# Kernel tuning notes

Measured on AMD Instinct MI355X. Metric: run time of the kernel, lower is better.

The kernel has to match this reference:

```python
import jax, jax.numpy as jnp
import numpy as np

B, S, D = 2, 4096, 2048
HQ, HK, HV = 32, 8, 8
H = max(HQ, HK, HV)
DK, DV = 64, 64
OUT = 2048
CHUNK = 64  # chunked-recurrent block size


def setup_inputs() -> dict:
    key = jax.random.key(0)
    k1, k2, k3 = jax.random.split(key, 3)
    x = jax.random.normal(k1, (B, S, D), dtype=jnp.float32)
    input_state = jnp.zeros((B, H * DK * DV), dtype=jnp.float32)
    qkv = HQ * DK + HK * DK + HV * DV  # 3072
    # Linear weights stored as [in, out]; equals torch weight.T so y = x @ W
    W_in = jax.random.normal(k2, (D, qkv), dtype=jnp.float32) * (D ** -0.5)
    W_out = jax.random.normal(k3, (H * DV, OUT), dtype=jnp.float32) * ((H * DV) ** -0.5)
    return {"x": x, "input_state": input_state, "W_in": W_in, "W_out": W_out}


def _linear_attention(q, k, v, S0):
    # q,k,v: [B,S,H,d]; S0: [B,H,DK,DV]
    nc = S // CHUNK
    # move chunk axis to front for lax.scan: [nc, B, CHUNK, H, d]
    qc = jnp.moveaxis(q.reshape(B, nc, CHUNK, H, DK), 1, 0)
    kc = jnp.moveaxis(k.reshape(B, nc, CHUNK, H, DK), 1, 0)
    vc = jnp.moveaxis(v.reshape(B, nc, CHUNK, H, DV), 1, 0)
    mask = jnp.tril(jnp.ones((CHUNK, CHUNK), dtype=bool))  # causal within chunk

    def step(Sstate, blk):
        qb, kb, vb = blk  # [B,C,H,d]
        A = jnp.einsum('bihd,bjhd->bhij', qb, kb)
        A = jnp.where(mask, A, jnp.zeros((), A.dtype))
        o = jnp.einsum('bhij,bjhd->bihd', A, vb) \
            + jnp.einsum('bihd,bhde->bihe', qb, Sstate)
        Sstate = Sstate + jnp.einsum('bjhd,bjhe->bhde', kb, vb)
        return Sstate, o

    Sf, o = jax.lax.scan(step, S0, (qc, kc, vc))
    o = jnp.moveaxis(o, 0, 1).reshape(B, S, H, DV)
    return o, Sf


def reference(x, input_state, W_in, W_out):
    proj = x @ W_in  # [B,S,3072]
    q, k, v = jnp.split(proj, [HQ * DK, HQ * DK + HK * DK], axis=-1)
    q = q.reshape(B, S, HQ, DK)
    k = k.reshape(B, S, HK, DK)
    v = v.reshape(B, S, HV, DV)
    # GQA: repeat kv heads up to num_heads = max(...)
    k = jnp.repeat(k, H // HK, axis=2)
    v = jnp.repeat(v, H // HV, axis=2)
    S0 = input_state.reshape(B, H, DK, DV)
    o, Sf = _linear_attention(q, k, v, S0)
    out = o.reshape(B, S, H * DV) @ W_out
    return out, Sf.reshape(B, H, DK * DV)
```

## Files before the change

kernel.cpp:

```cpp
#include <hip/hip_runtime.h>

typedef __bf16 bf16_t;
typedef __bf16 bf16x8 __attribute__((ext_vector_type(8)));
typedef __bf16 bf16x4 __attribute__((ext_vector_type(4)));
typedef float  f32x4  __attribute__((ext_vector_type(4)));

#define MFMA16(a,b,c) __builtin_amdgcn_mfma_f32_16x16x32_bf16((a),(b),(c),0,0,0)

__device__ __forceinline__ void gl_lds16(const void* g, void* l) {
    __builtin_amdgcn_global_load_lds(
        (__attribute__((address_space(1))) void*)(g),
        (__attribute__((address_space(3))) void*)(l),
        16, 0, 0);
}

static constexpr int S_TOT   = 8192;
static constexpr int D_IN    = 2048;
static constexpr int QKV     = 3072;
static constexpr int OUT_D   = 2048;
static constexpr int NCHUNK  = 64;

__global__ __launch_bounds__(256)
void cvt_f32_bf16(const float* __restrict__ in, bf16_t* __restrict__ out) {
    int i = blockIdx.x * 256 + threadIdx.x;
    f32x4 v = ((const f32x4*)in)[i];
    bf16x4 o;
    o[0] = (bf16_t)v[0]; o[1] = (bf16_t)v[1]; o[2] = (bf16_t)v[2]; o[3] = (bf16_t)v[3];
    ((bf16x4*)out)[i] = o;
}

__global__ __launch_bounds__(256)
void transpose_f32_bf16(const float* __restrict__ in, bf16_t* __restrict__ out, int R, int C) {
    __shared__ float tile[64][65];
    const int t  = threadIdx.x;
    const int r0 = blockIdx.y * 64, c0 = blockIdx.x * 64;
#pragma unroll
    for (int p = 0; p < 4; p++) {
        int row = p * 16 + (t >> 4);
        int col = (t & 15) * 4;
        f32x4 v = *(const f32x4*)&in[(size_t)(r0 + row) * C + c0 + col];
        tile[row][col + 0] = v[0]; tile[row][col + 1] = v[1];
        tile[row][col + 2] = v[2]; tile[row][col + 3] = v[3];
    }
    __syncthreads();
#pragma unroll
    for (int p = 0; p < 4; p++) {
        int oc  = p * 16 + (t >> 4);
        int orr = (t & 15) * 4;
        bf16x4 v;
        v[0] = (bf16_t)tile[orr + 0][oc]; v[1] = (bf16_t)tile[orr + 1][oc];
        v[2] = (bf16_t)tile[orr + 2][oc]; v[3] = (bf16_t)tile[orr + 3][oc];
        *(bf16x4*)&out[(size_t)(c0 + oc) * R + r0 + orr] = v;
    }
}

template<int OUT_BF16>
__global__ __launch_bounds__(256)
void gemm_bt(const bf16_t* __restrict__ A, const bf16_t* __restrict__ Bt,
             void* __restrict__ Cout, int M, int N, int K) {
    __shared__ alignas(16) bf16_t lA[128 * 32];
    __shared__ alignas(16) bf16_t lB[128 * 32];
    const int tid = threadIdx.x;
    const int m0 = blockIdx.y * 128;
    const int n0 = blockIdx.x * 128;
    const int w = tid >> 6, lane = tid & 63;
    const int wr = (w >> 1) * 64, wc = (w & 1) * 64;
    const int l15 = lane & 15, q8 = (lane >> 4) * 8, q4 = (lane >> 4) * 4;
    f32x4 acc[4][4] = {};
    const bf16_t* Ag = A + (size_t)(m0 + (tid >> 2)) * K + (tid & 3) * 8;
    const bf16_t* Bg = Bt + (size_t)(n0 + (tid >> 2)) * K + (tid & 3) * 8;
    const size_t rowStep = (size_t)64 * K;
    bf16_t* lA_t = lA + tid * 8;
    bf16_t* lB_t = lB + tid * 8;
    for (int k0 = 0; k0 < K; k0 += 32) {
        gl_lds16(Ag + k0,           lA_t);
        gl_lds16(Ag + k0 + rowStep, lA_t + 64 * 32);
        gl_lds16(Bg + k0,           lB_t);
        gl_lds16(Bg + k0 + rowStep, lB_t + 64 * 32);
        __syncthreads();
        bf16x8 af[4], bf_[4];
#pragma unroll
        for (int mi = 0; mi < 4; mi++) af[mi]  = *(const bf16x8*)&lA[(wr + mi * 16 + l15) * 32 + q8];
#pragma unroll
        for (int nj = 0; nj < 4; nj++) bf_[nj] = *(const bf16x8*)&lB[(wc + nj * 16 + l15) * 32 + q8];
#pragma unroll
        for (int mi = 0; mi < 4; mi++)
#pragma unroll
            for (int nj = 0; nj < 4; nj++)
                acc[mi][nj] = MFMA16(af[mi], bf_[nj], acc[mi][nj]);
        __syncthreads();
    }
    if (OUT_BF16) {
        bf16_t* C = (bf16_t*)Cout;
#pragma unroll
        for (int mi = 0; mi < 4; mi++)
#pragma unroll
            for (int nj = 0; nj < 4; nj++)
#pragma unroll
                for (int r = 0; r < 4; r++)
                    C[(size_t)(m0 + wr + mi * 16 + q4 + r) * N + n0 + wc + nj * 16 + l15] =
                        (bf16_t)acc[mi][nj][r];
    } else {
        float* C = (float*)Cout;
#pragma unroll
        for (int mi = 0; mi < 4; mi++)
#pragma unroll
            for (int nj = 0; nj < 4; nj++)
#pragma unroll
                for (int r = 0; r < 4; r++)
                    C[(size_t)(m0 + wr + mi * 16 + q4 + r) * N + n0 + wc + nj * 16 + l15] =
                        acc[mi][nj][r];
    }
}

__global__ __launch_bounds__(64)
void chunk_kv(const bf16_t* __restrict__ proj, float* __restrict__ Zc) {
    const int idx = blockIdx.x;
    const int c = idx & 63, hk = (idx >> 6) & 7, b = idx >> 9;
    const int tokBase = b * 4096 + c * 64;
    __shared__ alignas(16) bf16_t kT[64 * 64];
    __shared__ alignas(16) bf16_t vT[64 * 64];
    const int lane = threadIdx.x;
    const bf16_t* kg = proj + (size_t)tokBase * QKV + 2048 + hk * 64;
    const bf16_t* vg = proj + (size_t)tokBase * QKV + 2560 + hk * 64;
#pragma unroll
    for (int p = 0; p < 8; p++) {
        int tok = p * 8 + (lane >> 3);
        int d0  = (lane & 7) * 8;
        bf16x8 kv = *(const bf16x8*)&kg[(size_t)tok * QKV + d0];
        bf16x8 vv = *(const bf16x8*)&vg[(size_t)tok * QKV + d0];
#pragma unroll
        for (int e = 0; e < 8; e++) {
            kT[(d0 + e) * 64 + tok] = kv[e];
            vT[(d0 + e) * 64 + tok] = vv[e];
        }
    }
    __syncthreads();
    const int l15 = lane & 15, q8 = (lane >> 4) * 8, q4 = (lane >> 4) * 4;
    f32x4 acc[4][4] = {};
#pragma unroll
    for (int ks = 0; ks < 2; ks++) {
        bf16x8 af[4], bf_[4];
#pragma unroll
        for (int mi = 0; mi < 4; mi++) af[mi]  = *(const bf16x8*)&vT[(mi * 16 + l15) * 64 + ks * 32 + q8];
#pragma unroll
        for (int nj = 0; nj < 4; nj++) bf_[nj] = *(const bf16x8*)&kT[(nj * 16 + l15) * 64 + ks * 32 + q8];
#pragma unroll
        for (int mi = 0; mi < 4; mi++)
#pragma unroll
            for (int nj = 0; nj < 4; nj++)
                acc[mi][nj] = MFMA16(af[mi], bf_[nj], acc[mi][nj]);
    }
    float* zout = Zc + (size_t)idx * 4096;
#pragma unroll
    for (int mi = 0; mi < 4; mi++)
#pragma unroll
        for (int nj = 0; nj < 4; nj++)
#pragma unroll
            for (int r = 0; r < 4; r++)
                zout[(mi * 16 + q4 + r) * 64 + nj * 16 + l15] = acc[mi][nj][r];
}

__global__ __launch_bounds__(256)
void prefix_state(const float* __restrict__ Zc, const float* __restrict__ S0,
                  bf16_t* __restrict__ Zp, float* __restrict__ SfOut) {
    const int slice = blockIdx.x & 15;
    const int bh = blockIdx.x >> 4;
    const int h = bh & 31, b = bh >> 5;
    const int hk = h >> 2;
    const int e = slice * 256 + threadIdx.x;
    const int dv = e >> 6, dk = e & 63;
    float acc = S0[(size_t)b * 131072 + h * 4096 + dk * 64 + dv];
    const float* zc = Zc + ((size_t)(b * 8 + hk) * 64) * 4096 + e;
    bf16_t* zp = Zp + ((size_t)(b * 32 + h) * 64) * 4096 + e;
    for (int c = 0; c < NCHUNK; c++) {
        zp[(size_t)c * 4096] = (bf16_t)acc;
        acc += zc[(size_t)c * 4096];
    }
    SfOut[(size_t)b * 131072 + h * 4096 + dk * 64 + dv] = acc;
}

__global__ __launch_bounds__(64)
void attn_chunk(const bf16_t* __restrict__ proj, const bf16_t* __restrict__ Zp,
                bf16_t* __restrict__ O) {
    const int idx = blockIdx.x;
    const int g = idx & 3, hk = (idx >> 2) & 7, c = (idx >> 5) & 63, b = idx >> 11;
    const int h = hk * 4 + g;
    const int tokBase = b * 4096 + c * 64;
    __shared__ alignas(16) bf16_t q_lds[64 * 64];
    __shared__ alignas(16) bf16_t k_lds[64 * 64];
    __shared__ alignas(16) bf16_t vT[64 * 64];
    __shared__ alignas(16) bf16_t zs[64 * 64];
    const int lane = threadIdx.x;
    const bf16_t* qg = proj + (size_t)tokBase * QKV + h * 64;
    const bf16_t* kg = proj + (size_t)tokBase * QKV + 2048 + hk * 64;
    const bf16_t* zg = Zp + (((size_t)(b * 32 + h)) * 64 + c) * 4096;
#pragma unroll
    for (int p = 0; p < 8; p++) {
        int row = p * 8 + (lane >> 3);
        int col = (lane & 7) * 8;
        gl_lds16(&qg[(size_t)row * QKV + col], &q_lds[p * 512 + lane * 8]);
        gl_lds16(&kg[(size_t)row * QKV + col], &k_lds[p * 512 + lane * 8]);
        gl_lds16(&zg[p * 512 + lane * 8],      &zs[p * 512 + lane * 8]);
    }
    const bf16_t* vg = proj + (size_t)tokBase * QKV + 2560 + hk * 64;
#pragma unroll
    for (int p = 0; p < 8; p++) {
        int tok = p * 8 + (lane >> 3);
        int d0  = (lane & 7) * 8;
        bf16x8 vv = *(const bf16x8*)&vg[(size_t)tok * QKV + d0];
#pragma unroll
        for (int e = 0; e < 8; e++) vT[(d0 + e) * 64 + tok] = vv[e];
    }
    __syncthreads();
    const int l15 = lane & 15, q8 = (lane >> 4) * 8, q4 = (lane >> 4) * 4;
    bf16x8 qf[2][4];
#pragma unroll
    for (int ks = 0; ks < 2; ks++)
#pragma unroll
        for (int mi = 0; mi < 4; mi++)
            qf[ks][mi] = *(const bf16x8*)&q_lds[(mi * 16 + l15) * 64 + ks * 32 + q8];
    f32x4 oacc[4][4] = {};
#pragma unroll
    for (int ks = 0; ks < 2; ks++) {
        bf16x8 zf[4];
#pragma unroll
        for (int nj = 0; nj < 4; nj++) zf[nj] = *(const bf16x8*)&zs[(nj * 16 + l15) * 64 + ks * 32 + q8];
#pragma unroll
        for (int mi = 0; mi < 4; mi++)
#pragma unroll
            for (int nj = 0; nj < 4; nj++)
                oacc[mi][nj] = MFMA16(qf[ks][mi], zf[nj], oacc[mi][nj]);
    }
    f32x4 sacc[4][4] = {};
#pragma unroll
    for (int ks = 0; ks < 2; ks++) {
        bf16x8 kf[4];
#pragma unroll
        for (int nj = 0; nj < 4; nj++) kf[nj] = *(const bf16x8*)&k_lds[(nj * 16 + l15) * 64 + ks * 32 + q8];
#pragma unroll
        for (int mi = 0; mi < 4; mi++)
#pragma unroll
            for (int nj = 0; nj < 4; nj++)
                if (mi >= nj) sacc[mi][nj] = MFMA16(qf[ks][mi], kf[nj], sacc[mi][nj]);
    }
    __syncthreads();
#pragma unroll
    for (int mi = 0; mi < 4; mi++)
#pragma unroll
        for (int nj = 0; nj < 4; nj++)
#pragma unroll
            for (int r = 0; r < 4; r++) {
                int ti = mi * 16 + q4 + r, tj = nj * 16 + l15;
                float v = (ti >= tj) ? sacc[mi][nj][r] : 0.0f;
                zs[ti * 64 + tj] = (bf16_t)v;
            }
    __syncthreads();
#pragma unroll
    for (int ks = 0; ks < 2; ks++) {
        bf16x8 sf[4], vf[4];
#pragma unroll
        for (int mi = 0; mi < 4; mi++) sf[mi] = *(const bf16x8*)&zs[(mi * 16 + l15) * 64 + ks * 32 + q8];
#pragma unroll
        for (int nj = 0; nj < 4; nj++) vf[nj] = *(const bf16x8*)&vT[(nj * 16 + l15) * 64 + ks * 32 + q8];
#pragma unroll
        for (int mi = 0; mi < 4; mi++)
#pragma unroll
            for (int nj = 0; nj < 4; nj++)
                oacc[mi][nj] = MFMA16(sf[mi], vf[nj], oacc[mi][nj]);
    }
    bf16_t* og = O + (size_t)tokBase * OUT_D + h * 64;
#pragma unroll
    for (int mi = 0; mi < 4; mi++)
#pragma unroll
        for (int nj = 0; nj < 4; nj++)
#pragma unroll
            for (int r = 0; r < 4; r++)
                og[(size_t)(mi * 16 + q4 + r) * OUT_D + nj * 16 + l15] = (bf16_t)oacc[mi][nj][r];
}

extern "C" void kernel_launch(void* const* d_in, const int* in_sizes, int n_in,
                              void* d_out, int out_size, void* d_ws, size_t ws_size,
                              hipStream_t stream) {
    const float* x     = (const float*)d_in[0];
    const float* S0    = (const float*)d_in[1];
    const float* W_in  = (const float*)d_in[2];
    const float* W_out = (const float*)d_in[3];

    char* ws = (char*)d_ws;
    bf16_t* xb    = (bf16_t*)(ws + 0);
    bf16_t* WinT  = (bf16_t*)(ws + 33554432);
    bf16_t* WoutT = (bf16_t*)(ws + 46137344);
    bf16_t* proj  = (bf16_t*)(ws + 54525952);
    float*  Zc    = (float*) (ws + 104857600);
    bf16_t* Zp    = (bf16_t*)(ws + 121634816);
    bf16_t* Ob    = (bf16_t*)(ws + 0);

    float* outMain  = (float*)d_out;
    float* outState = (float*)d_out + (size_t)S_TOT * OUT_D;

    cvt_f32_bf16<<<16384, 256, 0, stream>>>(x, xb);
    transpose_f32_bf16<<<dim3(48, 32), 256, 0, stream>>>(W_in, WinT, 2048, 3072);
    transpose_f32_bf16<<<dim3(32, 32), 256, 0, stream>>>(W_out, WoutT, 2048, 2048);
    gemm_bt<1><<<dim3(24, 64), 256, 0, stream>>>(xb, WinT, proj, S_TOT, QKV, D_IN);
    chunk_kv<<<1024, 64, 0, stream>>>(proj, Zc);
    prefix_state<<<1024, 256, 0, stream>>>(Zc, S0, Zp, outState);
    attn_chunk<<<4096, 64, 0, stream>>>(proj, Zp, Ob);
    gemm_bt<0><<<dim3(16, 64), 256, 0, stream>>>(Ob, WoutT, outMain, S_TOT, OUT_D, OUT_D);
}
```

Before: 451.1 us.

## Precompute transposed K/V once and read attention operands directly from global

Adds a transpose_kv kernel that writes K^T and V^T per chunk to workspace, so chunk_kv and attn_chunk no longer transpose K/V in LDS. The 4x GQA redundancy of the V transpose in attn_chunk goes away. attn_chunk now loads Q, K, Z and V^T fragments straight from global memory instead of staging them through LDS, and it drops one barrier. The GEMM gets a min-occupancy launch bound and loads A fragments one at a time to reduce register pressure. This costs an extra kernel launch and extra global traffic, and the direct fragment loads from global are uncoalesced and may be slow.

```diff
diff --git a/kernel.cpp b/kernel.cpp
--- a/kernel.cpp
+++ b/kernel.cpp
@@ -55,7 +55,7 @@
 }
 
 template<int OUT_BF16>
-__global__ __launch_bounds__(256)
+__global__ __launch_bounds__(256, 4)
 void gemm_bt(const bf16_t* __restrict__ A, const bf16_t* __restrict__ Bt,
              void* __restrict__ Cout, int M, int N, int K) {
     __shared__ alignas(16) bf16_t lA[128 * 32];
@@ -78,16 +78,16 @@
         gl_lds16(Bg + k0,           lB_t);
         gl_lds16(Bg + k0 + rowStep, lB_t + 64 * 32);
         __syncthreads();
-        bf16x8 af[4], bf_[4];
-#pragma unroll
-        for (int mi = 0; mi < 4; mi++) af[mi]  = *(const bf16x8*)&lA[(wr + mi * 16 + l15) * 32 + q8];
-#pragma unroll
-        for (int nj = 0; nj < 4; nj++) bf_[nj] = *(const bf16x8*)&lB[(wc + nj * 16 + l15) * 32 + q8];
-#pragma unroll
-        for (int mi = 0; mi < 4; mi++)
-#pragma unroll
-            for (int nj = 0; nj < 4; nj++)
-                acc[mi][nj] = MFMA16(af[mi], bf_[nj], acc[mi][nj]);
+        bf16x8 bfr[4];
+#pragma unroll
+        for (int nj = 0; nj < 4; nj++) bfr[nj] = *(const bf16x8*)&lB[(wc + nj * 16 + l15) * 32 + q8];
+#pragma unroll
+        for (int mi = 0; mi < 4; mi++) {
+            bf16x8 afr = *(const bf16x8*)&lA[(wr + mi * 16 + l15) * 32 + q8];
+#pragma unroll
+            for (int nj = 0; nj < 4; nj++)
+                acc[mi][nj] = MFMA16(afr, bfr[nj], acc[mi][nj]);
+        }
         __syncthreads();
     }
     if (OUT_BF16) {
@@ -114,29 +114,47 @@
 }
 
 __global__ __launch_bounds__(64)
-void chunk_kv(const bf16_t* __restrict__ proj, float* __restrict__ Zc) {
+void transpose_kv(const bf16_t* __restrict__ proj,
+                  bf16_t* __restrict__ kT_g, bf16_t* __restrict__ vT_g) {
     const int idx = blockIdx.x;
     const int c = idx & 63, hk = (idx >> 6) & 7, b = idx >> 9;
     const int tokBase = b * 4096 + c * 64;
-    __shared__ alignas(16) bf16_t kT[64 * 64];
-    __shared__ alignas(16) bf16_t vT[64 * 64];
+    __shared__ float tile[64][65];
     const int lane = threadIdx.x;
-    const bf16_t* kg = proj + (size_t)tokBase * QKV + 2048 + hk * 64;
-    const bf16_t* vg = proj + (size_t)tokBase * QKV + 2560 + hk * 64;
-#pragma unroll
-    for (int p = 0; p < 8; p++) {
-        int tok = p * 8 + (lane >> 3);
-        int d0  = (lane & 7) * 8;
-        bf16x8 kv = *(const bf16x8*)&kg[(size_t)tok * QKV + d0];
-        bf16x8 vv = *(const bf16x8*)&vg[(size_t)tok * QKV + d0];
-#pragma unroll
-        for (int e = 0; e < 8; e++) {
-            kT[(d0 + e) * 64 + tok] = kv[e];
-            vT[(d0 + e) * 64 + tok] = vv[e];
+#pragma unroll
+    for (int which = 0; which < 2; which++) {
+        const bf16_t* src = proj + (size_t)tokBase * QKV + 2048 + which * 512 + hk * 64;
+        bf16_t* dst = (which ? vT_g : kT_g) + (size_t)idx * 4096;
+#pragma unroll
+        for (int p = 0; p < 8; p++) {
+            int tok = p * 8 + (lane >> 3);
+            int d0  = (lane & 7) * 8;
+            bf16x8 v = *(const bf16x8*)&src[(size_t)tok * QKV + d0];
+#pragma unroll
+            for (int e = 0; e < 8; e++) tile[tok][d0 + e] = (float)v[e];
         }
-    }
-    __syncthreads();
+        __syncthreads();
+#pragma unroll
+        for (int p = 0; p < 8; p++) {
+            int dk = p * 8 + (lane >> 3);
+            int t0 = (lane & 7) * 8;
+            bf16x8 o;
+#pragma unroll
+            for (int e = 0; e < 8; e++) o[e] = (bf16_t)tile[t0 + e][dk];
+            *(bf16x8*)&dst[dk * 64 + t0] = o;
+        }
+        __syncthreads();
+    }
+}
+
+__global__ __launch_bounds__(64)
+void chunk_kv(const bf16_t* __restrict__ kT_g, const bf16_t* __restrict__ vT_g,
+              float* __restrict__ Zc) {
+    const int idx = blockIdx.x;
+    const int lane = threadIdx.x;
     const int l15 = lane & 15, q8 = (lane >> 4) * 8, q4 = (lane >> 4) * 4;
+    const bf16_t* vT = vT_g + (size_t)idx * 4096;
+    const bf16_t* kT = kT_g + (size_t)idx * 4096;
     f32x4 acc[4][4] = {};
 #pragma unroll
     for (int ks = 0; ks < 2; ks++) {
@@ -181,51 +199,33 @@
 }
 
 __global__ __launch_bounds__(64)
-void attn_chunk(const bf16_t* __restrict__ proj, const bf16_t* __restrict__ Zp,
-                bf16_t* __restrict__ O) {
+void attn_chunk(const bf16_t* __restrict__ proj, const bf16_t* __restrict__ vT_g,
+                const bf16_t* __restrict__ Zp, bf16_t* __restrict__ O) {
     const int idx = blockIdx.x;
     const int g = idx & 3, hk = (idx >> 2) & 7, c = (idx >> 5) & 63, b = idx >> 11;
     const int h = hk * 4 + g;
     const int tokBase = b * 4096 + c * 64;
-    __shared__ alignas(16) bf16_t q_lds[64 * 64];
-    __shared__ alignas(16) bf16_t k_lds[64 * 64];
-    __shared__ alignas(16) bf16_t vT[64 * 64];
     __shared__ alignas(16) bf16_t zs[64 * 64];
     const int lane = threadIdx.x;
-    const bf16_t* qg = proj + (size_t)tokBase * QKV + h * 64;
-    const bf16_t* kg = proj + (size_t)tokBase * QKV + 2048 + hk * 64;
-    const bf16_t* zg = Zp + (((size_t)(b * 32 + h)) * 64 + c) * 4096;
-#pragma unroll
-    for (int p = 0; p < 8; p++) {
-        int row = p * 8 + (lane >> 3);
-        int col = (lane & 7) * 8;
-        gl_lds16(&qg[(size_t)row * QKV + col], &q_lds[p * 512 + lane * 8]);
-        gl_lds16(&kg[(size_t)row * QKV + col], &k_lds[p * 512 + lane * 8]);
-        gl_lds16(&zg[p * 512 + lane * 8],      &zs[p * 512 + lane * 8]);
-    }
-    const bf16_t* vg = proj + (size_t)tokBase * QKV + 2560 + hk * 64;
-#pragma unroll
-    for (int p = 0; p < 8; p++) {
-        int tok = p * 8 + (lane >> 3);
-        int d0  = (lane & 7) * 8;
-        bf16x8 vv = *(const bf16x8*)&vg[(size_t)tok * QKV + d0];
-#pragma unroll
-        for (int e = 0; e < 8; e++) vT[(d0 + e) * 64 + tok] = vv[e];
-    }
-    __syncthreads();
     const int l15 = lane & 15, q8 = (lane >> 4) * 8, q4 = (lane >> 4) * 4;
+    const bf16_t* qrow  = proj + (size_t)tokBase * QKV + h * 64;
+    const bf16_t* krow  = proj + (size_t)tokBase * QKV + 2048 + hk * 64;
+    const bf16_t* zrow  = Zp + (((size_t)(b * 32 + h)) * 64 + c) * 4096;
+    const bf16_t* vTrow = vT_g + ((size_t)(b * 8 + hk) * 64 + c) * 4096;
+
     bf16x8 qf[2][4];
 #pragma unroll
     for (int ks = 0; ks < 2; ks++)
 #pragma unroll
         for (int mi = 0; mi < 4; mi++)
-            qf[ks][mi] = *(const bf16x8*)&q_lds[(mi * 16 + l15) * 64 + ks * 32 + q8];
+            qf[ks][mi] = *(const bf16x8*)&qrow[(size_t)(mi * 16 + l15) * QKV + ks * 32 + q8];
+
     f32x4 oacc[4][4] = {};
 #pragma unroll
     for (int ks = 0; ks < 2; ks++) {
         bf16x8 zf[4];
 #pragma unroll
-        for (int nj = 0; nj < 4; nj++) zf[nj] = *(const bf16x8*)&zs[(nj * 16 + l15) * 64 + ks * 32 + q8];
+        for (int nj = 0; nj < 4; nj++) zf[nj] = *(const bf16x8*)&zrow[(nj * 16 + l15) * 64 + ks * 32 + q8];
 #pragma unroll
         for (int mi = 0; mi < 4; mi++)
 #pragma unroll
@@ -237,14 +237,13 @@
     for (int ks = 0; ks < 2; ks++) {
         bf16x8 kf[4];
 #pragma unroll
-        for (int nj = 0; nj < 4; nj++) kf[nj] = *(const bf16x8*)&k_lds[(nj * 16 + l15) * 64 + ks * 32 + q8];
+        for (int nj = 0; nj < 4; nj++) kf[nj] = *(const bf16x8*)&krow[(size_t)(nj * 16 + l15) * QKV + ks * 32 + q8];
 #pragma unroll
         for (int mi = 0; mi < 4; mi++)
 #pragma unroll
             for (int nj = 0; nj < 4; nj++)
                 if (mi >= nj) sacc[mi][nj] = MFMA16(qf[ks][mi], kf[nj], sacc[mi][nj]);
     }
-    __syncthreads();
 #pragma unroll
     for (int mi = 0; mi < 4; mi++)
 #pragma unroll
@@ -262,7 +261,7 @@
 #pragma unroll
         for (int mi = 0; mi < 4; mi++) sf[mi] = *(const bf16x8*)&zs[(mi * 16 + l15) * 64 + ks * 32 + q8];
 #pragma unroll
-        for (int nj = 0; nj < 4; nj++) vf[nj] = *(const bf16x8*)&vT[(nj * 16 + l15) * 64 + ks * 32 + q8];
+        for (int nj = 0; nj < 4; nj++) vf[nj] = *(const bf16x8*)&vTrow[(nj * 16 + l15) * 64 + ks * 32 + q8];
 #pragma unroll
         for (int mi = 0; mi < 4; mi++)
 #pragma unroll
@@ -289,7 +288,9 @@
 
     char* ws = (char*)d_ws;
     bf16_t* xb    = (bf16_t*)(ws + 0);
+    bf16_t* kT_g  = (bf16_t*)(ws + 16777216);
     bf16_t* WinT  = (bf16_t*)(ws + 33554432);
+    bf16_t* vT_g  = (bf16_t*)(ws + 33554432);
     bf16_t* WoutT = (bf16_t*)(ws + 46137344);
     bf16_t* proj  = (bf16_t*)(ws + 54525952);
     float*  Zc    = (float*) (ws + 104857600);
@@ -303,8 +304,9 @@
     transpose_f32_bf16<<<dim3(48, 32), 256, 0, stream>>>(W_in, WinT, 2048, 3072);
     transpose_f32_bf16<<<dim3(32, 32), 256, 0, stream>>>(W_out, WoutT, 2048, 2048);
     gemm_bt<1><<<dim3(24, 64), 256, 0, stream>>>(xb, WinT, proj, S_TOT, QKV, D_IN);
-    chunk_kv<<<1024, 64, 0, stream>>>(proj, Zc);
+    transpose_kv<<<1024, 64, 0, stream>>>(proj, kT_g, vT_g);
+    chunk_kv<<<1024, 64, 0, stream>>>(kT_g, vT_g, Zc);
     prefix_state<<<1024, 256, 0, stream>>>(Zc, S0, Zp, outState);
-    attn_chunk<<<4096, 64, 0, stream>>>(proj, Zp, Ob);
+    attn_chunk<<<4096, 64, 0, stream>>>(proj, vT_g, Zp, Ob);
     gemm_bt<0><<<dim3(16, 64), 256, 0, stream>>>(Ob, WoutT, outMain, S_TOT, OUT_D, OUT_D);
 }
```

Result: faster. 414.4 us (-8.1%).
